# Kernel tuning notes

Measured on AMD Instinct MI355X. Metric: run time of the kernel, lower is better.

The kernel has to match this reference:

```python
import jax, jax.numpy as jnp
import numpy as np

D_MODEL = 512
N_HEADS = 8
HEAD_DIM = D_MODEL // N_HEADS
SCALE = float(np.sqrt(HEAD_DIM))


def setup_inputs() -> dict:
    key = jax.random.key(0)
    k1, k2, k3, k4, k5, k6 = jax.random.split(key, 6)
    B, T, S = 4, 2048, 4096
    query = jax.random.normal(k1, (B, T, D_MODEL), dtype=jnp.float32)
    keys = jax.random.normal(k2, (B, S, D_MODEL), dtype=jnp.float32)
    key_padding_mask = jnp.zeros((B, S), dtype=bool)  # all valid
    # Linear params (torch nn.Linear: y = x @ W.T + b)
    lim = 1.0 / np.sqrt(D_MODEL)
    q_w = jax.random.uniform(k3, (D_MODEL, D_MODEL), jnp.float32, -lim, lim)
    q_b = jax.random.uniform(k4, (D_MODEL,), jnp.float32, -lim, lim)
    k_w = jax.random.uniform(k5, (D_MODEL, D_MODEL), jnp.float32, -lim, lim)
    k_b = jax.random.uniform(k6, (D_MODEL,), jnp.float32, -lim, lim)
    return {"query": query, "keys": keys, "key_padding_mask": key_padding_mask,
            "q_w": q_w, "q_b": q_b, "k_w": k_w, "k_b": k_b}


def reference(query, keys, key_padding_mask, q_w, q_b, k_w, k_b):
    B, T, _ = query.shape
    S = keys.shape[1]
    q = (query @ q_w.T + q_b).reshape(B, T, N_HEADS, HEAD_DIM)
    k = (keys @ k_w.T + k_b).reshape(B, S, N_HEADS, HEAD_DIM)
    # mean over heads of scaled per-head QK^T == single contraction over (h,d)
    # divided by n_heads*scale; avoids materializing [B,H,T,S].
    logits = jnp.einsum('bthd,bshd->bts', q, k) / (N_HEADS * SCALE)
    logits = jnp.where(key_padding_mask[:, None, :], -jnp.inf, logits)
    return logits
```

## Files before the change

### kernel.cpp

```cpp
#include <hip/hip_runtime.h>
#include <hip/hip_bf16.h>

using bf16 = __hip_bfloat16;
typedef __attribute__((ext_vector_type(8))) short short8;
typedef __attribute__((ext_vector_type(16))) float floatx16;

#define NEG_INF (-__builtin_huge_valf())

__device__ __forceinline__ void gld_lds16(const void* g, void* l) {
  __builtin_amdgcn_global_load_lds(
      (const __attribute__((address_space(1))) unsigned int*)g,
      (__attribute__((address_space(3))) unsigned int*)l, 16, 0, 0);
}

__device__ __forceinline__ void cvt8(const float4& a, const float4& b, bf16* t) {
  t[0] = __float2bfloat16(a.x); t[1] = __float2bfloat16(a.y);
  t[2] = __float2bfloat16(a.z); t[3] = __float2bfloat16(a.w);
  t[4] = __float2bfloat16(b.x); t[5] = __float2bfloat16(b.y);
  t[6] = __float2bfloat16(b.z); t[7] = __float2bfloat16(b.w);
}

__global__ void cvt_w(const float* __restrict__ qw, const float* __restrict__ kw,
                      bf16* __restrict__ qwo, bf16* __restrict__ kwo) {
  const int i = blockIdx.x * blockDim.x + threadIdx.x;
  const long e = (long)i << 3;
  const float* src = (e < 262144) ? qw + e : kw + (e - 262144);
  bf16*        dst = (e < 262144) ? qwo + e : kwo + (e - 262144);
  float4 a = *(const float4*)src;
  float4 b = *(const float4*)(src + 4);
  bf16 t[8];
  cvt8(a, b, t);
  *(short8*)dst = *(short8*)t;
}

__device__ __forceinline__ void mfma_tile32(const bf16* sAh, const bf16* sBh,
                                            int wm, int wn, int lane,
                                            floatx16 acc[2][2]) {
  const int fm = lane & 31;
  const int fk = (lane >> 5) * 8;
  #pragma unroll
  for (int ks = 0; ks < 2; ++ks) {
    short8 a0 = *(const short8*)(sAh + (wm +  0 + fm) * 32 + ks * 16 + fk);
    short8 a1 = *(const short8*)(sAh + (wm + 32 + fm) * 32 + ks * 16 + fk);
    short8 b0 = *(const short8*)(sBh + (wn +  0 + fm) * 32 + ks * 16 + fk);
    short8 b1 = *(const short8*)(sBh + (wn + 32 + fm) * 32 + ks * 16 + fk);
    acc[0][0] = __builtin_amdgcn_mfma_f32_32x32x16_bf16(a0, b0, acc[0][0], 0, 0, 0);
    acc[0][1] = __builtin_amdgcn_mfma_f32_32x32x16_bf16(a0, b1, acc[0][1], 0, 0, 0);
    acc[1][0] = __builtin_amdgcn_mfma_f32_32x32x16_bf16(a1, b0, acc[1][0], 0, 0, 0);
    acc[1][1] = __builtin_amdgcn_mfma_f32_32x32x16_bf16(a1, b1, acc[1][1], 0, 0, 0);
  }
}

__global__ __launch_bounds__(256) void proj_fused(const float* __restrict__ X,
                                                  const float* __restrict__ Y,
                                                  const bf16* __restrict__ qw,
                                                  const bf16* __restrict__ kw,
                                                  const float* __restrict__ qb,
                                                  const float* __restrict__ kb,
                                                  bf16* __restrict__ qo,
                                                  bf16* __restrict__ ko) {
  __shared__ bf16 sA[2][128 * 32];
  __shared__ bf16 sB[2][128 * 32];
  const int mt = blockIdx.x;
  const bool isQ = mt < 64;
  const float* A    = isQ ? X  : Y;
  const bf16*  W    = isQ ? qw : kw;
  const float* bias = isQ ? qb : kb;
  bf16* out         = isQ ? qo : ko;
  const int m0 = (isQ ? mt : mt - 64) * 128;
  const int n0 = blockIdx.y * 128;

  const int tid  = threadIdx.x;
  const int lane = tid & 63;
  const int w    = tid >> 6;
  const int wm   = (w >> 1) * 64;
  const int wn   = (w & 1) * 64;
  const int st_row = lane >> 2;
  const int st_col = (lane & 3) * 8;

  floatx16 acc[2][2];
  #pragma unroll
  for (int mi = 0; mi < 2; ++mi)
    #pragma unroll
    for (int ni = 0; ni < 2; ++ni)
      #pragma unroll
      for (int r = 0; r < 16; ++r)
        acc[mi][ni][r] = 0.f;

  for (int kt = 0; kt < 512; kt += 64) {
    #pragma unroll
    for (int h = 0; h < 2; ++h)
      #pragma unroll
      for (int j = 0; j < 2; ++j) {
        const int r = (w << 5) + (j << 4);
        const bf16* gb = W + (size_t)(n0 + r + st_row) * 512 + kt + h * 32 + st_col;
        gld_lds16(gb, &sB[h][r * 32]);
      }
    #pragma unroll
    for (int h = 0; h < 2; ++h)
      #pragma unroll
      for (int j = 0; j < 2; ++j) {
        const int row = (w << 5) + (j << 4) + st_row;
        const float* ga = A + (size_t)(m0 + row) * 512 + kt + h * 32 + st_col;
        float4 a0 = *(const float4*)ga;
        float4 a1 = *(const float4*)(ga + 4);
        bf16 ta[8];
        cvt8(a0, a1, ta);
        *(short8*)(&sA[h][row * 32 + st_col]) = *(short8*)ta;
      }
    __syncthreads();

    #pragma unroll
    for (int h = 0; h < 2; ++h)
      mfma_tile32(sA[h], sB[h], wm, wn, lane, acc);
    __syncthreads();
  }

  const int col = lane & 31;
  const int rhi = (lane >> 5) * 4;
  #pragma unroll
  for (int ni = 0; ni < 2; ++ni) {
    const int gn = n0 + wn + ni * 32 + col;
    const float b = bias[gn];
    #pragma unroll
    for (int mi = 0; mi < 2; ++mi) {
      #pragma unroll
      for (int reg = 0; reg < 16; ++reg) {
        const int row = (reg & 3) + 8 * (reg >> 2) + rhi;
        out[(size_t)(m0 + wm + mi * 32 + row) * 512 + gn] =
            __float2bfloat16(acc[mi][ni][reg] + b);
      }
    }
  }
}

__global__ __launch_bounds__(256) void qk_gemm(const bf16* __restrict__ Q,
                                               const bf16* __restrict__ Kp,
                                               const unsigned char* __restrict__ mask,
                                               float* __restrict__ out) {
  __shared__ bf16 sA[2][128 * 32];
  __shared__ bf16 sB[2][128 * 32];
  const int b = blockIdx.z;
  const bf16* A  = Q  + (size_t)b * 2048 * 512;
  const bf16* Bm = Kp + (size_t)b * 4096 * 512;
  float* ob = out + (size_t)b * 2048 * 4096;
  const unsigned char* mb = mask + (size_t)b * 4096;
  const int m0 = blockIdx.x * 128;
  const int n0 = blockIdx.y * 128;

  const int tid  = threadIdx.x;
  const int lane = tid & 63;
  const int w    = tid >> 6;
  const int wm   = (w >> 1) * 64;
  const int wn   = (w & 1) * 64;
  const int st_row = lane >> 2;
  const int st_col = (lane & 3) * 8;

  floatx16 acc[2][2];
  #pragma unroll
  for (int mi = 0; mi < 2; ++mi)
    #pragma unroll
    for (int ni = 0; ni < 2; ++ni)
      #pragma unroll
      for (int r = 0; r < 16; ++r)
        acc[mi][ni][r] = 0.f;

  for (int kt = 0; kt < 512; kt += 64) {
    #pragma unroll
    for (int h = 0; h < 2; ++h)
      #pragma unroll
      for (int j = 0; j < 2; ++j) {
        const int r = (w << 5) + (j << 4);
        const bf16* ga = A  + (size_t)(m0 + r + st_row) * 512 + kt + h * 32 + st_col;
        const bf16* gb = Bm + (size_t)(n0 + r + st_row) * 512 + kt + h * 32 + st_col;
        gld_lds16(ga, &sA[h][r * 32]);
        gld_lds16(gb, &sB[h][r * 32]);
      }
    __syncthreads();

    #pragma unroll
    for (int h = 0; h < 2; ++h)
      mfma_tile32(sA[h], sB[h], wm, wn, lane, acc);
    __syncthreads();
  }

  const int col = lane & 31;
  const int rhi = (lane >> 5) * 4;
  const float scale = 1.0f / 64.0f;
  #pragma unroll
  for (int ni = 0; ni < 2; ++ni) {
    const int gn = n0 + wn + ni * 32 + col;
    const bool msk = mb[gn] != 0;
    #pragma unroll
    for (int mi = 0; mi < 2; ++mi) {
      #pragma unroll
      for (int reg = 0; reg < 16; ++reg) {
        const int row = (reg & 3) + 8 * (reg >> 2) + rhi;
        ob[(size_t)(m0 + wm + mi * 32 + row) * 4096 + gn] =
            msk ? NEG_INF : acc[mi][ni][reg] * scale;
      }
    }
  }
}

extern "C" void kernel_launch(void* const* d_in, const int* in_sizes, int n_in,
                              void* d_out, int out_size, void* d_ws, size_t ws_size,
                              hipStream_t stream) {
  const float* query = (const float*)d_in[0];
  const float* keys  = (const float*)d_in[1];
  const unsigned char* mask = (const unsigned char*)d_in[2];
  const float* q_w = (const float*)d_in[3];
  const float* q_b = (const float*)d_in[4];
  const float* k_w = (const float*)d_in[5];
  const float* k_b = (const float*)d_in[6];
  float* out = (float*)d_out;

  const int B = 4, T = 2048, S = 4096, D = 512;
  const int nq = B * T * D;
  const int nk = B * S * D;
  const int nw = D * D;

  char* ws = (char*)d_ws;
  bf16* q_proj = (bf16*)(ws);
  bf16* k_proj = (bf16*)(ws + (size_t)nq * 2);
  bf16* qw_bf  = (bf16*)(ws + (size_t)(nq + nk) * 2);
  bf16* kw_bf  = (bf16*)(ws + (size_t)(nq + nk + nw) * 2);

  cvt_w<<<256, 256, 0, stream>>>(q_w, k_w, qw_bf, kw_bf);
  proj_fused<<<dim3(192, D / 128), 256, 0, stream>>>(query, keys, qw_bf, kw_bf,
                                                     q_b, k_b, q_proj, k_proj);
  qk_gemm<<<dim3(T / 128, S / 128, B), 256, 0, stream>>>(q_proj, k_proj, mask, out);
}
```

Measured before the change: 232.3 us.

## Fold key projection into query side via precomputed Wq^T Wk product

Rewrites logits as X·(Wq^T Wk)·Y^T plus rank-one bias terms. A new prep kernel computes the 512x512 combined matrix, the bias-weight vectors and the bias dot product. The query side now runs one GEMM against the combined matrix, while keys are only converted to bf16 and reduced into a per-row bias vector. This removes the key projection GEMM, the larger of the two projections. In exchange the prep kernel runs a serial FP32 GEMM on few blocks, and bf16 rounding of the combined matrix may change numerical error.

```diff
diff --git a/kernel.cpp b/kernel.cpp
--- a/kernel.cpp
+++ b/kernel.cpp
@@ -20,17 +20,90 @@
   t[6] = __float2bfloat16(b.z); t[7] = __float2bfloat16(b.w);
 }
 
-__global__ void cvt_w(const float* __restrict__ qw, const float* __restrict__ kw,
-                      bf16* __restrict__ qwo, bf16* __restrict__ kwo) {
-  const int i = blockIdx.x * blockDim.x + threadIdx.x;
-  const long e = (long)i << 3;
-  const float* src = (e < 262144) ? qw + e : kw + (e - 262144);
-  bf16*        dst = (e < 262144) ? qwo + e : kwo + (e - 262144);
-  float4 a = *(const float4*)src;
-  float4 b = *(const float4*)(src + 4);
-  bf16 t[8];
-  cvt8(a, b, t);
-  *(short8*)dst = *(short8*)t;
+
+__global__ __launch_bounds__(256) void prep(const float* __restrict__ qw,
+                                            const float* __restrict__ kw,
+                                            const float* __restrict__ qb,
+                                            const float* __restrict__ kb,
+                                            bf16* __restrict__ mtp,
+                                            float* __restrict__ w1,
+                                            float* __restrict__ w2,
+                                            float* __restrict__ cks) {
+  __shared__ float pool[2][2][8][64];
+  const int bid = blockIdx.x;
+  const int tid = threadIdx.x;
+
+  if (bid < 64) {
+    float (*skw)[8][64] = pool[0];
+    float (*sqw)[8][64] = pool[1];
+    const int n0 = (bid >> 3) * 64, k0 = (bid & 7) * 64;
+    const int tr = tid >> 4, tc = tid & 15;
+    const int sr = tid >> 5, sc = (tid & 31) * 2;
+    float acc[4][4];
+    #pragma unroll
+    for (int x = 0; x < 4; ++x)
+      #pragma unroll
+      for (int y = 0; y < 4; ++y) acc[x][y] = 0.f;
+
+    auto stage = [&](int buf, int i0) {
+      float2 kv = *(const float2*)&kw[(size_t)(i0 + sr) * 512 + n0 + sc];
+      float2 qv = *(const float2*)&qw[(size_t)(i0 + sr) * 512 + k0 + sc];
+      skw[buf][sr][sc] = kv.x; skw[buf][sr][sc + 1] = kv.y;
+      sqw[buf][sr][sc] = qv.x; sqw[buf][sr][sc + 1] = qv.y;
+    };
+    stage(0, 0);
+    __syncthreads();
+    for (int cb = 0; cb < 64; ++cb) {
+      if (cb < 63) stage((cb + 1) & 1, (cb + 1) * 8);
+      const int buf = cb & 1;
+      #pragma unroll
+      for (int ii = 0; ii < 8; ++ii) {
+        float av[4], bv[4];
+        #pragma unroll
+        for (int x = 0; x < 4; ++x) av[x] = skw[buf][ii][tr * 4 + x];
+        #pragma unroll
+        for (int y = 0; y < 4; ++y) bv[y] = sqw[buf][ii][tc * 4 + y];
+        #pragma unroll
+        for (int x = 0; x < 4; ++x)
+          #pragma unroll
+          for (int y = 0; y < 4; ++y) acc[x][y] += av[x] * bv[y];
+      }
+      __syncthreads();
+    }
+    #pragma unroll
+    for (int x = 0; x < 4; ++x)
+      #pragma unroll
+      for (int y = 0; y < 4; ++y)
+        mtp[(size_t)(n0 + tr * 4 + x) * 512 + k0 + tc * 4 + y] =
+            __float2bfloat16(acc[x][y]);
+  } else {
+    const int bid2 = bid - 64;
+    const bool isW1 = bid2 < 8;
+    const float* src = isW1 ? qw : kw;
+    const float* vec = isW1 ? kb : qb;
+    float* outp      = isW1 ? w1 : w2;
+    const int j = ((bid2 & 7) << 6) | (tid & 63);
+    const int q = tid >> 6;
+    float p = 0.f;
+    #pragma unroll 8
+    for (int i = q * 128; i < q * 128 + 128; ++i)
+      p += src[(size_t)i * 512 + j] * vec[i];
+    float* red = &pool[0][0][0][0];
+    red[tid] = p;
+    __syncthreads();
+    if (tid < 64)
+      outp[j] = red[tid] + red[tid + 64] + red[tid + 128] + red[tid + 192];
+    if (bid2 == 0) {
+      __syncthreads();
+      red[tid] = qb[tid] * kb[tid] + qb[tid + 256] * kb[tid + 256];
+      __syncthreads();
+      for (int s = 128; s > 0; s >>= 1) {
+        if (tid < s) red[tid] += red[tid + s];
+        __syncthreads();
+      }
+      if (tid == 0) *cks = red[0];
+    }
+  }
 }
 
 __device__ __forceinline__ void mfma_tile32(const bf16* sAh, const bf16* sBh,
@@ -51,24 +124,17 @@
   }
 }
 
-__global__ __launch_bounds__(256) void proj_fused(const float* __restrict__ X,
-                                                  const float* __restrict__ Y,
-                                                  const bf16* __restrict__ qw,
-                                                  const bf16* __restrict__ kw,
-                                                  const float* __restrict__ qb,
-                                                  const float* __restrict__ kb,
-                                                  bf16* __restrict__ qo,
-                                                  bf16* __restrict__ ko) {
+__global__ __launch_bounds__(256) void proj_z(const float* __restrict__ X,
+                                              const bf16* __restrict__ Mt,
+                                              const float* __restrict__ w1,
+                                              const float* __restrict__ cks,
+                                              bf16* __restrict__ Z,
+                                              float* __restrict__ u) {
   __shared__ bf16 sA[2][128 * 32];
   __shared__ bf16 sB[2][128 * 32];
-  const int mt = blockIdx.x;
-  const bool isQ = mt < 64;
-  const float* A    = isQ ? X  : Y;
-  const bf16*  W    = isQ ? qw : kw;
-  const float* bias = isQ ? qb : kb;
-  bf16* out         = isQ ? qo : ko;
-  const int m0 = (isQ ? mt : mt - 64) * 128;
+  const int m0 = blockIdx.x * 128;
   const int n0 = blockIdx.y * 128;
+  const bool doU = (blockIdx.y == 0);
 
   const int tid  = threadIdx.x;
   const int lane = tid & 63;
@@ -87,26 +153,35 @@
       for (int r = 0; r < 16; ++r)
         acc[mi][ni][r] = 0.f;
 
+  float pu[2] = {0.f, 0.f};
+
   for (int kt = 0; kt < 512; kt += 64) {
     #pragma unroll
     for (int h = 0; h < 2; ++h)
       #pragma unroll
       for (int j = 0; j < 2; ++j) {
         const int r = (w << 5) + (j << 4);
-        const bf16* gb = W + (size_t)(n0 + r + st_row) * 512 + kt + h * 32 + st_col;
-        gld_lds16(gb, &sB[h][r * 32]);
+        gld_lds16(Mt + (size_t)(n0 + r + st_row) * 512 + kt + h * 32 + st_col,
+                  &sB[h][r * 32]);
       }
     #pragma unroll
     for (int h = 0; h < 2; ++h)
       #pragma unroll
       for (int j = 0; j < 2; ++j) {
         const int row = (w << 5) + (j << 4) + st_row;
-        const float* ga = A + (size_t)(m0 + row) * 512 + kt + h * 32 + st_col;
+        const float* ga = X + (size_t)(m0 + row) * 512 + kt + h * 32 + st_col;
         float4 a0 = *(const float4*)ga;
         float4 a1 = *(const float4*)(ga + 4);
         bf16 ta[8];
         cvt8(a0, a1, ta);
         *(short8*)(&sA[h][row * 32 + st_col]) = *(short8*)ta;
+        if (doU) {
+          const float* wv = w1 + kt + h * 32 + st_col;
+          float4 wa = *(const float4*)wv;
+          float4 wb = *(const float4*)(wv + 4);
+          pu[j] += a0.x * wa.x + a0.y * wa.y + a0.z * wa.z + a0.w * wa.w +
+                   a1.x * wb.x + a1.y * wb.y + a1.z * wb.z + a1.w * wb.w;
+        }
       }
     __syncthreads();
 
@@ -114,6 +189,18 @@
     for (int h = 0; h < 2; ++h)
       mfma_tile32(sA[h], sB[h], wm, wn, lane, acc);
     __syncthreads();
+  }
+
+  if (doU) {
+    const float c = *cks;
+    #pragma unroll
+    for (int j = 0; j < 2; ++j) {
+      float p = pu[j];
+      p += __shfl_xor(p, 1, 64);
+      p += __shfl_xor(p, 2, 64);
+      if ((lane & 3) == 0)
+        u[m0 + (w << 5) + (j << 4) + st_row] = p + c;
+    }
   }
 
   const int col = lane & 31;
@@ -121,22 +208,46 @@
   #pragma unroll
   for (int ni = 0; ni < 2; ++ni) {
     const int gn = n0 + wn + ni * 32 + col;
-    const float b = bias[gn];
-    #pragma unroll
-    for (int mi = 0; mi < 2; ++mi) {
+    #pragma unroll
+    for (int mi = 0; mi < 2; ++mi)
       #pragma unroll
       for (int reg = 0; reg < 16; ++reg) {
         const int row = (reg & 3) + 8 * (reg >> 2) + rhi;
-        out[(size_t)(m0 + wm + mi * 32 + row) * 512 + gn] =
-            __float2bfloat16(acc[mi][ni][reg] + b);
-      }
-    }
-  }
+        Z[(size_t)(m0 + wm + mi * 32 + row) * 512 + gn] =
+            __float2bfloat16(acc[mi][ni][reg]);
+      }
+  }
+}
+
+__global__ __launch_bounds__(256) void yconv(const float* __restrict__ k,
+                                             const float* __restrict__ w2,
+                                             bf16* __restrict__ ko,
+                                             float* __restrict__ v) {
+  const size_t e = ((size_t)blockIdx.x * 256 + threadIdx.x) * 8;
+  const float* src = k + e;
+  bf16*        dst = ko + e;
+  const float* wv  = w2 + (int)(e & 511);
+
+  float4 a = *(const float4*)src;
+  float4 c = *(const float4*)(src + 4);
+  bf16 t[8];
+  cvt8(a, c, t);
+  *(short8*)dst = *(short8*)t;
+
+  float4 wa = *(const float4*)wv;
+  float4 wb = *(const float4*)(wv + 4);
+  float p = a.x * wa.x + a.y * wa.y + a.z * wa.z + a.w * wa.w +
+            c.x * wb.x + c.y * wb.y + c.z * wb.z + c.w * wb.w;
+  #pragma unroll
+  for (int d = 1; d < 64; d <<= 1) p += __shfl_xor(p, d, 64);
+  if ((threadIdx.x & 63) == 0) v[e >> 9] = p;
 }
 
 __global__ __launch_bounds__(256) void qk_gemm(const bf16* __restrict__ Q,
                                                const bf16* __restrict__ Kp,
                                                const unsigned char* __restrict__ mask,
+                                               const float* __restrict__ u,
+                                               const float* __restrict__ v,
                                                float* __restrict__ out) {
   __shared__ bf16 sA[2][128 * 32];
   __shared__ bf16 sB[2][128 * 32];
@@ -145,6 +256,8 @@
   const bf16* Bm = Kp + (size_t)b * 4096 * 512;
   float* ob = out + (size_t)b * 2048 * 4096;
   const unsigned char* mb = mask + (size_t)b * 4096;
+  const float* ub = u + (size_t)b * 2048;
+  const float* vb = v + (size_t)b * 4096;
   const int m0 = blockIdx.x * 128;
   const int n0 = blockIdx.y * 128;
 
@@ -191,13 +304,15 @@
   for (int ni = 0; ni < 2; ++ni) {
     const int gn = n0 + wn + ni * 32 + col;
     const bool msk = mb[gn] != 0;
+    const float vc = vb[gn];
     #pragma unroll
     for (int mi = 0; mi < 2; ++mi) {
       #pragma unroll
       for (int reg = 0; reg < 16; ++reg) {
         const int row = (reg & 3) + 8 * (reg >> 2) + rhi;
-        ob[(size_t)(m0 + wm + mi * 32 + row) * 4096 + gn] =
-            msk ? NEG_INF : acc[mi][ni][reg] * scale;
+        const int gm = m0 + wm + mi * 32 + row;
+        ob[(size_t)gm * 4096 + gn] =
+            msk ? NEG_INF : (acc[mi][ni][reg] + ub[gm] + vc) * scale;
       }
     }
   }
@@ -215,19 +330,18 @@
   const float* k_b = (const float*)d_in[6];
   float* out = (float*)d_out;
 
-  const int B = 4, T = 2048, S = 4096, D = 512;
-  const int nq = B * T * D;
-  const int nk = B * S * D;
-  const int nw = D * D;
-
   char* ws = (char*)d_ws;
-  bf16* q_proj = (bf16*)(ws);
-  bf16* k_proj = (bf16*)(ws + (size_t)nq * 2);
-  bf16* qw_bf  = (bf16*)(ws + (size_t)(nq + nk) * 2);
-  bf16* kw_bf  = (bf16*)(ws + (size_t)(nq + nk + nw) * 2);
-
-  cvt_w<<<256, 256, 0, stream>>>(q_w, k_w, qw_bf, kw_bf);
-  proj_fused<<<dim3(192, D / 128), 256, 0, stream>>>(query, keys, qw_bf, kw_bf,
-                                                     q_b, k_b, q_proj, k_proj);
-  qk_gemm<<<dim3(T / 128, S / 128, B), 256, 0, stream>>>(q_proj, k_proj, mask, out);
-}
+  bf16*  mt_bf = (bf16*)(ws);
+  bf16*  z_bf  = (bf16*)(ws + 524288);
+  bf16*  y_bf  = (bf16*)(ws + 8912896);
+  float* u     = (float*)(ws + 25690112);
+  float* v     = (float*)(ws + 25722880);
+  float* w1    = (float*)(ws + 25788416);
+  float* w2    = (float*)(ws + 25790464);
+  float* cks   = (float*)(ws + 25792512);
+
+  prep<<<80, 256, 0, stream>>>(q_w, k_w, q_b, k_b, mt_bf, w1, w2, cks);
+  proj_z<<<dim3(64, 4), 256, 0, stream>>>(query, mt_bf, w1, cks, z_bf, u);
+  yconv<<<4096, 256, 0, stream>>>(keys, w2, y_bf, v);
+  qk_gemm<<<dim3(16, 32, 4), 256, 0, stream>>>(z_bf, y_bf, mask, u, v, out);
+}
```

New measurement: 314.6 us. +35.4%, slower.
